# Performance work log

Hardware: AMD Instinct MI355X
Metric: run time of the kernel (lower is better)

The kernel has to match this reference:

```python
import jax, jax.numpy as jnp
import numpy as np

NTOKEN = 100000
NINP = 64
N_EDGES = 600000
BATCH = 64
MAX_LEN = 200


def gcn_conv(x, W, b, edge_index, num_nodes):
    # PyG GCNConv: add self-loops, symmetric normalization, x @ W then propagate.
    src, dst = edge_index[0], edge_index[1]
    loop = jnp.arange(num_nodes, dtype=src.dtype)
    src = jnp.concatenate([src, loop])
    dst = jnp.concatenate([dst, loop])
    deg = jax.ops.segment_sum(jnp.ones_like(dst, dtype=x.dtype), dst,
                              num_segments=num_nodes)
    dinv = jnp.where(deg > 0, deg ** -0.5, 0.0)
    norm = dinv[src] * dinv[dst]                      # [E+N]
    h = x @ W                                         # [N, out]
    out = jax.ops.segment_sum(h[src] * norm[:, None], dst,
                              num_segments=num_nodes)  # [N, out]
    return out + b


def setup_inputs() -> dict:
    key = jax.random.key(0)
    k_emb, k_w1, k_w2, k_e, k_in = jax.random.split(key, 5)
    # Xavier-normal scaled params
    emb = jax.random.normal(k_emb, (NTOKEN, NINP), jnp.float32) * (2.0 / (NTOKEN + NINP)) ** 0.5
    emb = emb.at[0].set(0.0)  # padding_idx=0
    W1 = jax.random.normal(k_w1, (NINP, 2 * NINP), jnp.float32) * (2.0 / (3 * NINP)) ** 0.5
    b1 = jnp.zeros((2 * NINP,), jnp.float32)
    W2 = jax.random.normal(k_w2, (2 * NINP, NINP), jnp.float32) * (2.0 / (3 * NINP)) ** 0.5
    b2 = jnp.zeros((NINP,), jnp.float32)
    edge_index = jax.random.randint(k_e, (2, N_EDGES), 0, NTOKEN, dtype=jnp.int32)
    inp = jax.random.randint(k_in, (BATCH, MAX_LEN), 0, NTOKEN, dtype=jnp.int32)
    return {"input": inp, "emb": emb, "W1": W1, "b1": b1,
            "W2": W2, "b2": b2, "edge_index": edge_index}


def reference(input, emb, W1, b1, W2, b2, edge_index):
    # GraphNN forward (eval mode: dropout = identity, no activation between convs)
    h = gcn_conv(emb, W1, b1, edge_index, NTOKEN)          # [N, 2*ninp]
    lookup = gcn_conv(h, W2, b2, edge_index, NTOKEN)       # [N, ninp]
    # one-hot scatter + einsum('bt,td->bd') is exactly a row gather:
    out = lookup[input]                                    # [B, L, ninp]
    return out
```

## Files before the change

kernel.cpp:

```cpp
#include <hip/hip_runtime.h>
#include <hip/hip_fp16.h>
#include <math.h>

static constexpr int NTOK = 100000;
static constexpr int NE   = 600000;
static constexpr int NPOS = 64 * 200;
static constexpr int NBKT = 196;
static constexpr int BCAP = 5120;
static constexpr int EPB  = 2344;
static constexpr int EPT  = 10;

typedef unsigned long long ull;

__device__ __forceinline__ float2 h2f(unsigned int u) {
    __half2 h = *reinterpret_cast<__half2*>(&u);
    return __half22float2(h);
}
__device__ __forceinline__ unsigned int f2h(float a, float b) {
    __half2 h = __floats2half2_rn(a, b);
    return *reinterpret_cast<unsigned int*>(&h);
}
__device__ __forceinline__ float u16f(unsigned short x) {
    __half h = *reinterpret_cast<__half*>(&x);
    return __half2float(h);
}

__global__ void k_setup(const float4* __restrict__ W14, const float* __restrict__ b1,
                        const float4* __restrict__ W24, float4* __restrict__ W124,
                        float4* __restrict__ bw4, int* __restrict__ bucketCnt,
                        const float4* __restrict__ emb4, uint4* __restrict__ embh4) {
    int t = threadIdx.x;
    if (blockIdx.x < 4) {
        int j4 = t & 15;
        int k = blockIdx.x * 16 + (t >> 4);
        float4 acc = {0.f, 0.f, 0.f, 0.f};
        for (int mq = 0; mq < 32; ++mq) {
            float4 a = W14[k * 32 + mq];
            float4 w0 = W24[(4 * mq + 0) * 16 + j4];
            float4 w1 = W24[(4 * mq + 1) * 16 + j4];
            float4 w2 = W24[(4 * mq + 2) * 16 + j4];
            float4 w3 = W24[(4 * mq + 3) * 16 + j4];
            acc.x += a.x * w0.x + a.y * w1.x + a.z * w2.x + a.w * w3.x;
            acc.y += a.x * w0.y + a.y * w1.y + a.z * w2.y + a.w * w3.y;
            acc.z += a.x * w0.z + a.y * w1.z + a.z * w2.z + a.w * w3.z;
            acc.w += a.x * w0.w + a.y * w1.w + a.z * w2.w + a.w * w3.w;
        }
        W124[k * 16 + j4] = acc;
        if (blockIdx.x == 0 && t < 16) {
            float4 b = {0.f, 0.f, 0.f, 0.f};
            for (int m = 0; m < 128; ++m) {
                float a = b1[m];
                float4 w = W24[m * 16 + t];
                b.x += a * w.x; b.y += a * w.y; b.z += a * w.z; b.w += a * w.w;
            }
            bw4[t] = b;
        }
    } else if (blockIdx.x == 4) {
        bucketCnt[t] = 0;
    } else {
        int i = (blockIdx.x - 5) * 256 + t;
        if (i < NTOK * 8) {
            float4 a = emb4[2 * i];
            float4 b = emb4[2 * i + 1];
            uint4 o;
            o.x = f2h(a.x, a.y); o.y = f2h(a.z, a.w);
            o.z = f2h(b.x, b.y); o.w = f2h(b.z, b.w);
            embh4[i] = o;
        }
    }
}

__global__ __launch_bounds__(256) void
k_bucket(const int* __restrict__ ei, int* __restrict__ bucketCnt,
         ull* __restrict__ buckets) {
    __shared__ int cnt[256];
    __shared__ int pref[256];
    __shared__ int eoff[256];
    __shared__ int base[256];
    __shared__ ull stg[EPB];
    int t = threadIdx.x;
    cnt[t] = 0;
    __syncthreads();

    int e0 = blockIdx.x * EPB;
    int eEnd = e0 + EPB; if (eEnd > NE) eEnd = NE;
    int tot = eEnd - e0;

    int s_[EPT], d_[EPT], r_[EPT];
#pragma unroll
    for (int k = 0; k < EPT; ++k) {
        int i = e0 + t + k * 256;
        s_[k] = -1;
        if (i < eEnd) {
            s_[k] = ei[i];
            d_[k] = ei[NE + i];
            r_[k] = atomicAdd(&cnt[d_[k] >> 9], 1);
        }
    }
    __syncthreads();

    int v = cnt[t];
    pref[t] = v;
    __syncthreads();
    for (int o = 1; o < 256; o <<= 1) {
        int x = pref[t];
        if (t >= o) x += pref[t - o];
        __syncthreads();
        pref[t] = x;
        __syncthreads();
    }
    eoff[t] = pref[t] - v;
    base[t] = (v > 0) ? atomicAdd(&bucketCnt[t], v) : 0;
    __syncthreads();

#pragma unroll
    for (int k = 0; k < EPT; ++k) {
        if (s_[k] >= 0) {
            int b = d_[k] >> 9;
            stg[eoff[b] + r_[k]] =
                ((ull)(unsigned)s_[k] << 32) | (unsigned)d_[k];
        }
    }
    __syncthreads();

    for (int i = t; i < tot; i += 256) {
        ull e = stg[i];
        int b = ((int)(unsigned)e) >> 9;
        int off = base[b] + (i - eoff[b]);
        if (off < BCAP) buckets[(long)b * BCAP + off] = e;
    }
}

__global__ __launch_bounds__(256) void
k_csrbuild(const ull* __restrict__ buckets, const int* __restrict__ bucketCnt,
           int* __restrict__ csr, int* __restrict__ roff, int* __restrict__ degs,
           float* __restrict__ dinv, float* __restrict__ dinv2) {
    __shared__ int cnt[512];
    __shared__ int pref[512];
    __shared__ int cur[512];
    __shared__ int bsum[256];
    __shared__ int stg[BCAP];
    int t = threadIdx.x;
    cnt[t] = 0; cnt[t + 256] = 0;
    __syncthreads();

    int b = blockIdx.x;
    int n0 = b << 9;
    int m = bucketCnt[b]; if (m > BCAP) m = BCAP;
    const ull* bb = buckets + (long)b * BCAP;

    for (int i = t; i < m; i += 256) {
        int dd = (int)(unsigned)bb[i];
        atomicAdd(&cnt[dd - n0], 1);
    }
    __syncthreads();

    int a0 = cnt[2 * t], a1 = cnt[2 * t + 1];
    bsum[t] = a0 + a1;
    __syncthreads();
    for (int o = 1; o < 256; o <<= 1) {
        int x = bsum[t];
        if (t >= o) x += bsum[t - o];
        __syncthreads();
        bsum[t] = x;
        __syncthreads();
    }
    int eb = bsum[t] - (a0 + a1);
    pref[2 * t] = eb;          cur[2 * t] = eb;
    pref[2 * t + 1] = eb + a0; cur[2 * t + 1] = eb + a0;
    __syncthreads();

    for (int i = t; i < m; i += 256) {
        ull v = bb[i];
        int dd = (int)(unsigned)v;
        int ss = (int)(v >> 32);
        int pos = atomicAdd(&cur[dd - n0], 1);
        stg[pos] = ss;
    }
    __syncthreads();

    for (int i = t; i < m; i += 256) csr[(long)b * BCAP + i] = stg[i];

#pragma unroll
    for (int k = 0; k < 2; ++k) {
        int l = t + k * 256;
        int n = n0 + l;
        if (n < NTOK) {
            int dg = cnt[l];
            degs[n] = dg;
            roff[n] = b * BCAP + pref[l];
            float dd = rsqrtf((float)dg + 1.0f);
            dinv[n] = dd;
            dinv2[n] = dd * dd;
        }
    }
}

__global__ void k_gatherA(const int* __restrict__ csr, const int* __restrict__ roff,
                          const int* __restrict__ degs,
                          const float* __restrict__ dinv, const uint4* __restrict__ eh4,
                          uint4* __restrict__ u4, float* __restrict__ s_raw) {
    int idx = blockIdx.x * 256 + threadIdx.x;
    int n = idx >> 3;
    if (n >= NTOK) return;
    int jq = idx & 7;
    int d = degs[n];
    const int* row = csr + roff[n];

    float a[8];
    float cn = dinv[n];
    {
        uint4 v = eh4[((long)n << 3) + jq];
        float2 f0 = h2f(v.x), f1 = h2f(v.y), f2 = h2f(v.z), f3 = h2f(v.w);
        a[0] = cn * f0.x; a[1] = cn * f0.y; a[2] = cn * f1.x; a[3] = cn * f1.y;
        a[4] = cn * f2.x; a[5] = cn * f2.y; a[6] = cn * f3.x; a[7] = cn * f3.y;
    }
    float sdv = cn;
    int e = 0;
    for (; e + 4 <= d; e += 4) {
        int s0 = row[e], s1 = row[e + 1], s2 = row[e + 2], s3 = row[e + 3];
        float c0 = dinv[s0], c1 = dinv[s1], c2 = dinv[s2], c3 = dinv[s3];
        uint4 v0 = eh4[((long)s0 << 3) + jq];
        uint4 v1 = eh4[((long)s1 << 3) + jq];
        uint4 v2 = eh4[((long)s2 << 3) + jq];
        uint4 v3 = eh4[((long)s3 << 3) + jq];
        {
            float2 f0 = h2f(v0.x), f1 = h2f(v0.y), f2 = h2f(v0.z), f3 = h2f(v0.w);
            a[0] += c0 * f0.x; a[1] += c0 * f0.y; a[2] += c0 * f1.x; a[3] += c0 * f1.y;
            a[4] += c0 * f2.x; a[5] += c0 * f2.y; a[6] += c0 * f3.x; a[7] += c0 * f3.y;
        }
        {
            float2 f0 = h2f(v1.x), f1 = h2f(v1.y), f2 = h2f(v1.z), f3 = h2f(v1.w);
            a[0] += c1 * f0.x; a[1] += c1 * f0.y; a[2] += c1 * f1.x; a[3] += c1 * f1.y;
            a[4] += c1 * f2.x; a[5] += c1 * f2.y; a[6] += c1 * f3.x; a[7] += c1 * f3.y;
        }
        {
            float2 f0 = h2f(v2.x), f1 = h2f(v2.y), f2 = h2f(v2.z), f3 = h2f(v2.w);
            a[0] += c2 * f0.x; a[1] += c2 * f0.y; a[2] += c2 * f1.x; a[3] += c2 * f1.y;
            a[4] += c2 * f2.x; a[5] += c2 * f2.y; a[6] += c2 * f3.x; a[7] += c2 * f3.y;
        }
        {
            float2 f0 = h2f(v3.x), f1 = h2f(v3.y), f2 = h2f(v3.z), f3 = h2f(v3.w);
            a[0] += c3 * f0.x; a[1] += c3 * f0.y; a[2] += c3 * f1.x; a[3] += c3 * f1.y;
            a[4] += c3 * f2.x; a[5] += c3 * f2.y; a[6] += c3 * f3.x; a[7] += c3 * f3.y;
        }
        sdv += (c0 + c1) + (c2 + c3);
    }
    for (; e < d; ++e) {
        int sx = row[e];
        float c = dinv[sx];
        uint4 v = eh4[((long)sx << 3) + jq];
        float2 f0 = h2f(v.x), f1 = h2f(v.y), f2 = h2f(v.z), f3 = h2f(v.w);
        a[0] += c * f0.x; a[1] += c * f0.y; a[2] += c * f1.x; a[3] += c * f1.y;
        a[4] += c * f2.x; a[5] += c * f2.y; a[6] += c * f3.x; a[7] += c * f3.y;
        sdv += c;
    }
    uint4 o;
    o.x = f2h(a[0], a[1]); o.y = f2h(a[2], a[3]);
    o.z = f2h(a[4], a[5]); o.w = f2h(a[6], a[7]);
    u4[((long)n << 3) + jq] = o;
    if (jq == 0) s_raw[n] = sdv;
}

__global__ __launch_bounds__(256) void
k_fused(const int* __restrict__ inp, const int* __restrict__ csr,
        const int* __restrict__ roff, const int* __restrict__ degs,
        const float* __restrict__ dinv, const float* __restrict__ dinv2,
        const float* __restrict__ s_raw, const unsigned short* __restrict__ uh,
        const float* __restrict__ W12, const float* __restrict__ bw,
        const float* __restrict__ b2, float* __restrict__ out) {
    __shared__ float w[64 * 64];
    int tid = threadIdx.x;
    {
        const float4* W4 = (const float4*)W12;
        float4* w4 = (float4*)w;
        for (int i = tid; i < 1024; i += 256) w4[i] = W4[i];
    }
    __syncthreads();

    int lane = tid & 63;
    int wid  = tid >> 6;
    int p = blockIdx.x * 4 + wid;
    int t = inp[p];
    int d = degs[t];
    const int* row = csr + roff[t];

    float z = dinv2[t] * u16f(uh[((long)t << 6) + lane]);
    int e = 0;
    for (; e + 4 <= d; e += 4) {
        int s0 = row[e], s1 = row[e + 1], s2 = row[e + 2], s3 = row[e + 3];
        float c0 = dinv2[s0], c1 = dinv2[s1], c2 = dinv2[s2], c3 = dinv2[s3];
        float u0 = u16f(uh[((long)s0 << 6) + lane]);
        float u1 = u16f(uh[((long)s1 << 6) + lane]);
        float u2 = u16f(uh[((long)s2 << 6) + lane]);
        float u3 = u16f(uh[((long)s3 << 6) + lane]);
        z += (c0 * u0 + c1 * u1) + (c2 * u2 + c3 * u3);
    }
    for (; e < d; ++e) {
        int sx = row[e];
        z += dinv2[sx] * u16f(uh[((long)sx << 6) + lane]);
    }
    z *= dinv[t];

    float o0 = 0.f, o1 = 0.f, o2 = 0.f, o3 = 0.f;
#pragma unroll
    for (int k = 0; k < 64; k += 4) {
        float z0 = __uint_as_float(__builtin_amdgcn_readlane(__float_as_uint(z), k));
        float z1 = __uint_as_float(__builtin_amdgcn_readlane(__float_as_uint(z), k + 1));
        float z2 = __uint_as_float(__builtin_amdgcn_readlane(__float_as_uint(z), k + 2));
        float z3 = __uint_as_float(__builtin_amdgcn_readlane(__float_as_uint(z), k + 3));
        o0 += z0 * w[(k + 0) * 64 + lane];
        o1 += z1 * w[(k + 1) * 64 + lane];
        o2 += z2 * w[(k + 2) * 64 + lane];
        o3 += z3 * w[(k + 3) * 64 + lane];
    }
    float o = (o0 + o1) + (o2 + o3) + dinv[t] * s_raw[t] * bw[lane] + b2[lane];
    out[((long)p << 6) + lane] = o;
}

extern "C" void kernel_launch(void* const* d_in, const int* in_sizes, int n_in,
                              void* d_out, int out_size, void* d_ws, size_t ws_size,
                              hipStream_t stream) {
    const int*   inp = (const int*)d_in[0];
    const float* emb = (const float*)d_in[1];
    const float* W1  = (const float*)d_in[2];
    const float* b1  = (const float*)d_in[3];
    const float* W2  = (const float*)d_in[4];
    const float* b2  = (const float*)d_in[5];
    const int*   ei  = (const int*)d_in[6];
    float* out = (float*)d_out;

    char* ws = (char*)d_ws;
    int*   bucketCnt = (int*)(ws + 0);
    float* W12   = (float*)(ws + 4096);
    float* bw    = (float*)(ws + 20480);
    int*   degs  = (int*)(ws + 24576);
    float* dinv  = (float*)(ws + 424576);
    float* dinv2 = (float*)(ws + 824576);
    float* s_raw = (float*)(ws + 1224576);
    int*   roff  = (int*)(ws + 1624576);
    ull*   buckets = (ull*)(ws + 2024576);
    int*   csr   = (int*)(ws + 10052736);
    unsigned short* embh = (unsigned short*)(ws + 14066816);
    unsigned short* u    = (unsigned short*)(ws + 26866816);

    k_setup<<<5 + (NTOK * 8 + 255) / 256, 256, 0, stream>>>(
        (const float4*)W1, b1, (const float4*)W2, (float4*)W12, (float4*)bw,
        bucketCnt, (const float4*)emb, (uint4*)embh);

    k_bucket<<<256, 256, 0, stream>>>(ei, bucketCnt, buckets);

    k_csrbuild<<<NBKT, 256, 0, stream>>>(buckets, bucketCnt, csr, roff,
                                         degs, dinv, dinv2);

    int gblk = (NTOK * 8 + 255) / 256;
    k_gatherA<<<gblk, 256, 0, stream>>>(csr, roff, degs, dinv, (const uint4*)embh,
                                        (uint4*)u, s_raw);

    k_fused<<<NPOS / 4, 256, 0, stream>>>(inp, csr, roff, degs, dinv, dinv2,
                                          s_raw, u, W12, bw, b2, out);
}
```

Before: 71.68 us.

## Restrict first-layer aggregation to nodes reachable from queried tokens

Adds a marking pass that flags every input token and its in-neighbours, then compacts the flags into a worklist so the first GCN gather runs only on nodes the second layer actually reads. The fp16 embedding conversion moves from k_setup into extra blocks of the CSR-build kernel so it overlaps with CSR construction. This skips first-layer work for unused nodes but adds two small kernels, scattered flag writes, and an atomic-based compaction. The gather grid is still sized for all nodes, so surplus threads exit early after reading the worklist count.

Measured after the change: 97.76 us. 1.36x slower.

```diff
diff --git a/kernel.cpp b/kernel.cpp
--- a/kernel.cpp
+++ b/kernel.cpp
@@ -28,7 +28,7 @@
 __global__ void k_setup(const float4* __restrict__ W14, const float* __restrict__ b1,
                         const float4* __restrict__ W24, float4* __restrict__ W124,
                         float4* __restrict__ bw4, int* __restrict__ bucketCnt,
-                        const float4* __restrict__ emb4, uint4* __restrict__ embh4) {
+                        int* __restrict__ wl_n, int* __restrict__ flagU) {
     int t = threadIdx.x;
     if (blockIdx.x < 4) {
         int j4 = t & 15;
@@ -57,16 +57,10 @@
         }
     } else if (blockIdx.x == 4) {
         bucketCnt[t] = 0;
+        if (t == 0) wl_n[0] = 0;
     } else {
         int i = (blockIdx.x - 5) * 256 + t;
-        if (i < NTOK * 8) {
-            float4 a = emb4[2 * i];
-            float4 b = emb4[2 * i + 1];
-            uint4 o;
-            o.x = f2h(a.x, a.y); o.y = f2h(a.z, a.w);
-            o.z = f2h(b.x, b.y); o.w = f2h(b.z, b.w);
-            embh4[i] = o;
-        }
+        if (i < NTOK) flagU[i] = 0;
     }
 }
 
@@ -134,13 +128,28 @@
 __global__ __launch_bounds__(256) void
 k_csrbuild(const ull* __restrict__ buckets, const int* __restrict__ bucketCnt,
            int* __restrict__ csr, int* __restrict__ roff, int* __restrict__ degs,
-           float* __restrict__ dinv, float* __restrict__ dinv2) {
+           float* __restrict__ dinv, float* __restrict__ dinv2,
+           const float4* __restrict__ emb4, uint4* __restrict__ embh4) {
     __shared__ int cnt[512];
     __shared__ int pref[512];
     __shared__ int cur[512];
     __shared__ int bsum[256];
     __shared__ int stg[BCAP];
     int t = threadIdx.x;
+
+    if (blockIdx.x >= NBKT) {
+        int i = (blockIdx.x - NBKT) * 256 + t;
+        if (i < NTOK * 8) {
+            float4 a = emb4[2 * i];
+            float4 b = emb4[2 * i + 1];
+            uint4 o;
+            o.x = f2h(a.x, a.y); o.y = f2h(a.z, a.w);
+            o.z = f2h(b.x, b.y); o.w = f2h(b.z, b.w);
+            embh4[i] = o;
+        }
+        return;
+    }
+
     cnt[t] = 0; cnt[t + 256] = 0;
     __syncthreads();
 
@@ -196,13 +205,43 @@
     }
 }
 
-__global__ void k_gatherA(const int* __restrict__ csr, const int* __restrict__ roff,
+__global__ void k_mark(const int* __restrict__ inp, const int* __restrict__ csr,
+                       const int* __restrict__ roff, const int* __restrict__ degs,
+                       int* __restrict__ flagU) {
+    int p = blockIdx.x * 256 + threadIdx.x;
+    if (p >= NPOS) return;
+    int t = inp[p];
+    flagU[t] = 1;
+    int d = degs[t];
+    const int* row = csr + roff[t];
+    for (int e = 0; e < d; ++e) flagU[row[e]] = 1;
+}
+
+__global__ void k_compact(const int* __restrict__ flagU, int* __restrict__ wl,
+                          int* __restrict__ wl_n) {
+    int n = blockIdx.x * 256 + threadIdx.x;
+    int lane = threadIdx.x & 63;
+    int f = (n < NTOK) ? flagU[n] : 0;
+    unsigned long long m = __ballot(f != 0);
+    int cw = __popcll(m);
+    int base = 0;
+    if (lane == 0 && cw) base = atomicAdd(wl_n, cw);
+    base = __builtin_amdgcn_readfirstlane(base);
+    if (f) {
+        int pos = base + __popcll(m & ((1ULL << lane) - 1));
+        wl[pos] = n;
+    }
+}
+
+__global__ void k_gatherA(const int* __restrict__ wl, const int* __restrict__ wl_n,
+                          const int* __restrict__ csr, const int* __restrict__ roff,
                           const int* __restrict__ degs,
                           const float* __restrict__ dinv, const uint4* __restrict__ eh4,
                           uint4* __restrict__ u4, float* __restrict__ s_raw) {
     int idx = blockIdx.x * 256 + threadIdx.x;
-    int n = idx >> 3;
-    if (n >= NTOK) return;
+    int wi = idx >> 3;
+    if (wi >= wl_n[0]) return;
+    int n = wl[wi];
     int jq = idx & 7;
     int d = degs[n];
     const int* row = csr + roff[n];
@@ -339,23 +378,30 @@
     float* dinv2 = (float*)(ws + 824576);
     float* s_raw = (float*)(ws + 1224576);
     int*   roff  = (int*)(ws + 1624576);
-    ull*   buckets = (ull*)(ws + 2024576);
-    int*   csr   = (int*)(ws + 10052736);
-    unsigned short* embh = (unsigned short*)(ws + 14066816);
-    unsigned short* u    = (unsigned short*)(ws + 26866816);
-
-    k_setup<<<5 + (NTOK * 8 + 255) / 256, 256, 0, stream>>>(
+    int*   flagU = (int*)(ws + 2024576);
+    int*   wl    = (int*)(ws + 2424576);
+    int*   wl_n  = (int*)(ws + 2824576);
+    ull*   buckets = (ull*)(ws + 2824592);
+    int*   csr   = (int*)(ws + 10852752);
+    unsigned short* embh = (unsigned short*)(ws + 14866832);
+    unsigned short* u    = (unsigned short*)(ws + 27666832);
+
+    k_setup<<<5 + (NTOK + 255) / 256, 256, 0, stream>>>(
         (const float4*)W1, b1, (const float4*)W2, (float4*)W12, (float4*)bw,
-        bucketCnt, (const float4*)emb, (uint4*)embh);
+        bucketCnt, wl_n, flagU);
 
     k_bucket<<<256, 256, 0, stream>>>(ei, bucketCnt, buckets);
 
-    k_csrbuild<<<NBKT, 256, 0, stream>>>(buckets, bucketCnt, csr, roff,
-                                         degs, dinv, dinv2);
+    k_csrbuild<<<NBKT + (NTOK * 8 + 255) / 256, 256, 0, stream>>>(
+        buckets, bucketCnt, csr, roff, degs, dinv, dinv2,
+        (const float4*)emb, (uint4*)embh);
+
+    k_mark<<<(NPOS + 255) / 256, 256, 0, stream>>>(inp, csr, roff, degs, flagU);
+    k_compact<<<(NTOK + 255) / 256, 256, 0, stream>>>(flagU, wl, wl_n);
 
     int gblk = (NTOK * 8 + 255) / 256;
-    k_gatherA<<<gblk, 256, 0, stream>>>(csr, roff, degs, dinv, (const uint4*)embh,
-                                        (uint4*)u, s_raw);
+    k_gatherA<<<gblk, 256, 0, stream>>>(wl, wl_n, csr, roff, degs, dinv,
+                                        (const uint4*)embh, (uint4*)u, s_raw);
 
     k_fused<<<NPOS / 4, 256, 0, stream>>>(inp, csr, roff, degs, dinv, dinv2,
                                           s_raw, u, W12, bw, b2, out);
```
